# Kernel optimization log

Hardware: AMD Instinct MI355X
Metric: run time of the kernel (lower is better)

The kernel has to match this reference:

```python
import jax, jax.numpy as jnp
import numpy as np


def _scan(xs, w, shift):
    """Sequential IRNN scan.
    xs: [L, B, C, K] - scan over leading axis L.
    shift: 0 = straight scan; +1 = previous line shifted right along K
    (diagonal toward increasing K); -1 = shifted left.
    First line is passed through unchanged (matches torch in-place code).
    """
    def step(carry, row):
        if shift == 0:
            new = jax.nn.relu(carry * w + row)
        elif shift == 1:
            new = jnp.concatenate(
                [row[..., :1], jax.nn.relu(carry[..., :-1] * w + row[..., 1:])], axis=-1)
        else:  # shift == -1
            new = jnp.concatenate(
                [jax.nn.relu(carry[..., 1:] * w + row[..., :-1]), row[..., -1:]], axis=-1)
        return new, new
    _, ys = jax.lax.scan(step, xs[0], xs[1:])
    return jnp.concatenate([xs[:1], ys], axis=0)


def setup_inputs() -> dict:
    key = jax.random.key(0)
    B, C, H, W = 8, 32, 256, 256
    x = jax.random.normal(key, (B, C, H, W), dtype=jnp.float32)
    one = jnp.float32(1.0)
    return {"x": x, "w_up": one, "w_down": one, "w_left": one, "w_right": one}


def reference(x, w_up, w_down, w_left, w_right):
    # Row-major view: [H, B, C, W]
    x_rows = jnp.moveaxis(x, 2, 0)
    top_down = jnp.moveaxis(_scan(x_rows, w_down, 0), 0, 2)
    top_up = jnp.moveaxis(
        jnp.flip(_scan(jnp.flip(x_rows, 0), w_up, 0), 0), 0, 2)
    # Diagonals use w_down, faithful to the original source (which reuses
    # self.down_weight for all four diagonal scans).
    top_zuoxia = jnp.moveaxis(_scan(x_rows, w_down, 1), 0, 2)
    top_youxia = jnp.moveaxis(_scan(x_rows, w_down, -1), 0, 2)

    # Column-major view: [W, B, C, H]
    x_cols = jnp.moveaxis(x, 3, 0)
    top_right = jnp.moveaxis(_scan(x_cols, w_right, 0), 0, 3)
    top_left = jnp.moveaxis(
        jnp.flip(_scan(jnp.flip(x_cols, 0), w_left, 0), 0), 0, 3)
    top_zuoshang = jnp.moveaxis(_scan(x_cols, w_down, 1), 0, 3)
    top_youshang = jnp.moveaxis(_scan(x_cols, w_down, -1), 0, 3)

    return (top_up, top_right, top_down, top_left,
            top_zuoxia, top_youxia, top_zuoshang, top_youshang)
```

## Files before the change

kernel.cpp:

```cpp
#include <hip/hip_runtime.h>


namespace {
constexpr int HH = 256;
constexpr int WW = 256;
constexpr int PLANE = HH * WW;
constexpr size_t TEN = (size_t)PLANE * 256;

__device__ __forceinline__ float relu_f(float a) { return fmaxf(a, 0.0f); }

typedef float v4f __attribute__((ext_vector_type(4)));

__device__ __forceinline__ void nt_store4(float* p, const float4& v) {
    v4f t; t.x = v.x; t.y = v.y; t.z = v.z; t.w = v.w;
    __builtin_nontemporal_store(t, (v4f*)p);
}

__device__ __forceinline__ float4 ld4(const float* p) { return *(const float4*)p; }

template <typename F>
__device__ __forceinline__ void scan_fwd(const float* xp, F&& step) {
    float4 buf[8];
    #pragma unroll
    for (int k = 0; k < 8; ++k) buf[k] = ld4(xp + (1 + k) * WW);
    #pragma unroll 1
    for (int g = 0; g < 30; ++g) {
        #pragma unroll
        for (int k = 0; k < 8; ++k) {
            const int r = 1 + 8 * g + k;
            float4 v = buf[k];
            buf[k] = ld4(xp + (r + 8) * WW);
            step(r, v);
        }
    }
    float4 t7[7];
    #pragma unroll
    for (int k = 0; k < 7; ++k) t7[k] = ld4(xp + (249 + k) * WW);
    #pragma unroll
    for (int k = 0; k < 8; ++k) step(241 + k, buf[k]);
    #pragma unroll
    for (int k = 0; k < 7; ++k) step(249 + k, t7[k]);
}

template <typename F>
__device__ __forceinline__ void scan_bwd(const float* xp, F&& step) {
    float4 buf[8];
    #pragma unroll
    for (int k = 0; k < 8; ++k) buf[k] = ld4(xp + (254 - k) * WW);
    #pragma unroll 1
    for (int g = 0; g < 30; ++g) {
        #pragma unroll
        for (int k = 0; k < 8; ++k) {
            const int h = 254 - (8 * g + k);
            float4 v = buf[k];
            buf[k] = ld4(xp + (h - 8) * WW);
            step(h, v);
        }
    }
    float4 t7[7];
    #pragma unroll
    for (int k = 0; k < 7; ++k) t7[k] = ld4(xp + (6 - k) * WW);
    #pragma unroll
    for (int k = 0; k < 8; ++k) step(14 - k, buf[k]);
    #pragma unroll
    for (int k = 0; k < 7; ++k) step(6 - k, t7[k]);
}
}

__global__ __launch_bounds__(64) void irnn_vertical(
    const float* __restrict__ x, float* __restrict__ out,
    const float* __restrict__ wup_p, const float* __restrict__ wdn_p)
{
    const int bid = blockIdx.x;
    const int t = threadIdx.x;

    if (bid < 256) {
        const int plane = bid;
        const float wd = *wdn_p;
        const float* xp = x + (size_t)plane * PLANE + t * 4;
        float* o2 = out + 2 * TEN + (size_t)plane * PLANE + t * 4;
        float* o4 = out + 4 * TEN + (size_t)plane * PLANE + t * 4;
        float* o5 = out + 5 * TEN + (size_t)plane * PLANE + t * 4;
        float* o6 = out + 6 * TEN + (size_t)plane * PLANE + t * 4;

        float4 c2 = ld4(xp);
        float4 c4 = c2, c5 = c2;
        nt_store4(o2, c2);
        nt_store4(o4, c4);
        nt_store4(o6, c4);
        nt_store4(o5, c5);

        scan_fwd(xp, [&](int r, float4 v) {
            c2.x = relu_f(c2.x * wd + v.x);
            c2.y = relu_f(c2.y * wd + v.y);
            c2.z = relu_f(c2.z * wd + v.z);
            c2.w = relu_f(c2.w * wd + v.w);
            nt_store4(o2 + r * WW, c2);
            {
                float pw = __shfl_up(c4.w, 1);
                float4 n;
                n.x = (t == 0) ? v.x : relu_f(pw * wd + v.x);
                n.y = relu_f(c4.x * wd + v.y);
                n.z = relu_f(c4.y * wd + v.z);
                n.w = relu_f(c4.z * wd + v.w);
                nt_store4(o4 + r * WW, n);
                nt_store4(o6 + r * WW, n);
                c4 = n;
            }
            {
                float nx = __shfl_down(c5.x, 1);
                float4 n;
                n.x = relu_f(c5.y * wd + v.x);
                n.y = relu_f(c5.z * wd + v.y);
                n.z = relu_f(c5.w * wd + v.z);
                n.w = (t == 63) ? v.w : relu_f(nx * wd + v.w);
                nt_store4(o5 + r * WW, n);
                c5 = n;
            }
        });
    } else {
        const int plane = bid - 256;
        const float wu = *wup_p;
        const float wd = *wdn_p;
        const float* xp = x + (size_t)plane * PLANE + t * 4;
        float* o0 = out + 0 * TEN + (size_t)plane * PLANE + t * 4;
        float* o7 = out + 7 * TEN + (size_t)plane * PLANE + t * 4;

        float4 c0 = ld4(xp + 255 * WW);
        float4 c7 = c0;
        nt_store4(o0 + 255 * WW, c0);
        nt_store4(o7 + 255 * WW, c7);

        scan_bwd(xp, [&](int h, float4 v) {
            c0.x = relu_f(c0.x * wu + v.x);
            c0.y = relu_f(c0.y * wu + v.y);
            c0.z = relu_f(c0.z * wu + v.z);
            c0.w = relu_f(c0.w * wu + v.w);
            nt_store4(o0 + h * WW, c0);
            {
                float pw = __shfl_up(c7.w, 1);
                float4 n;
                n.x = (t == 0) ? v.x : relu_f(pw * wd + v.x);
                n.y = relu_f(c7.x * wd + v.y);
                n.z = relu_f(c7.y * wd + v.z);
                n.w = relu_f(c7.z * wd + v.w);
                nt_store4(o7 + h * WW, n);
                c7 = n;
            }
        });
    }
}

__global__ __launch_bounds__(64) void irnn_horizontal(
    const float* __restrict__ x, float* __restrict__ out,
    const float* __restrict__ wlf_p, const float* __restrict__ wrt_p)
{
    __shared__ float xs[64][33];
    __shared__ float os[64][33];

    const int bid = blockIdx.x;
    const int dir = bid >> 10;
    const int rb  = bid & 1023;
    const size_t row0 = (size_t)rb * 64;
    const int t = threadIdx.x;
    const int lrow = t >> 3;
    const int lcol = (t & 7) * 4;

    const float w = dir ? *wlf_p : *wrt_p;
    float* op = out + (size_t)(dir ? 3 : 1) * TEN;

    float carry = 0.0f;
    for (int ci = 0; ci < 8; ++ci) {
        const int cw = dir ? (7 - ci) : ci;
        const int wbase = cw * 32;

        for (int p = 0; p < 8; ++p) {
            const int r = p * 8 + lrow;
            float4 v = *(const float4*)(x + (row0 + r) * WW + wbase + lcol);
            *(float4*)&xs[r][lcol] = v;
        }
        __syncthreads();

        if (dir == 0) {
            for (int j = 0; j < 32; ++j) {
                const float v = xs[t][j];
                const int wg = wbase + j;
                const float o = (wg == 0) ? v : relu_f(carry * w + v);
                carry = o;
                os[t][j] = o;
            }
        } else {
            for (int j = 31; j >= 0; --j) {
                const float v = xs[t][j];
                const int wg = wbase + j;
                const float o = (wg == WW - 1) ? v : relu_f(carry * w + v);
                carry = o;
                os[t][j] = o;
            }
        }
        __syncthreads();

        for (int p = 0; p < 8; ++p) {
            const int r = p * 8 + lrow;
            float4 v = *(const float4*)&os[r][lcol];
            nt_store4(op + (row0 + r) * WW + wbase + lcol, v);
        }
        __syncthreads();
    }
}

extern "C" void kernel_launch(void* const* d_in, const int* in_sizes, int n_in,
                              void* d_out, int out_size, void* d_ws, size_t ws_size,
                              hipStream_t stream) {
    const float* x      = (const float*)d_in[0];
    const float* w_up   = (const float*)d_in[1];
    const float* w_down = (const float*)d_in[2];
    const float* w_left = (const float*)d_in[3];
    const float* w_right= (const float*)d_in[4];
    float* out = (float*)d_out;

    hipLaunchKernelGGL(irnn_vertical, dim3(512), dim3(64), 0, stream,
                       x, out, w_up, w_down);
    hipLaunchKernelGGL(irnn_horizontal, dim3(2 * 1024), dim3(64), 0, stream,
                       x, out, w_left, w_right);
}
```

Before: 118.5 us.

## Fuse horizontal scans into vertical kernel via wave-level parallel prefix scan

Removes the separate horizontal kernel and computes left/right row scans inside the backward vertical blocks, using a lane-parallel prefix scan over each row built from composed affine-ReLU operators exchanged by shuffles. This avoids a second pass reading x and a second launch with shared-memory transposes. In exchange each row step gains many shuffles and extra ALU work on a latency-bound loop, and only 512 single-wave blocks carry all the work.

```diff
diff --git a/kernel.cpp b/kernel.cpp
--- a/kernel.cpp
+++ b/kernel.cpp
@@ -65,11 +65,84 @@
     #pragma unroll
     for (int k = 0; k < 7; ++k) step(6 - k, t7[k]);
 }
-}
-
-__global__ __launch_bounds__(64) void irnn_vertical(
+
+__device__ __forceinline__ float4 wscan_right(float4 v, float k, int t) {
+    float L, K, B;
+    if (t == 0) {
+        float o1 = relu_f(k * v.x + v.y);
+        float o2 = relu_f(k * o1 + v.z);
+        float o3 = relu_f(k * o2 + v.w);
+        L = o3; K = 0.0f; B = o3;
+    } else {
+        L = 0.0f; K = k; B = v.x;
+        L = fmaxf(0.0f, k * L + v.y); B = k * B + v.y; K = k * K;
+        L = fmaxf(0.0f, k * L + v.z); B = k * B + v.z; K = k * K;
+        L = fmaxf(0.0f, k * L + v.w); B = k * B + v.w; K = k * K;
+    }
+    #pragma unroll
+    for (int d = 1; d < 64; d <<= 1) {
+        float Lp = __shfl_up(L, d);
+        float Kp = __shfl_up(K, d);
+        float Bp = __shfl_up(B, d);
+        if (t >= d) {
+            float nL = fmaxf(L, K * Lp + B);
+            float nB = K * Bp + B;
+            float nK = K * Kp;
+            L = nL; B = nB; K = nK;
+        }
+    }
+    float Le = __shfl_up(L, 1);
+    float Be = __shfl_up(B, 1);
+    float c  = fmaxf(Le, Be);
+    float4 o;
+    o.x = (t == 0) ? v.x : relu_f(k * c + v.x);
+    o.y = relu_f(k * o.x + v.y);
+    o.z = relu_f(k * o.y + v.z);
+    o.w = relu_f(k * o.z + v.w);
+    return o;
+}
+
+__device__ __forceinline__ float4 wscan_left(float4 v, float k, int t) {
+    float L, K, B;
+    if (t == 63) {
+        float o2 = relu_f(k * v.w + v.z);
+        float o1 = relu_f(k * o2 + v.y);
+        float o0 = relu_f(k * o1 + v.x);
+        L = o0; K = 0.0f; B = o0;
+    } else {
+        L = 0.0f; K = k; B = v.w;
+        L = fmaxf(0.0f, k * L + v.z); B = k * B + v.z; K = k * K;
+        L = fmaxf(0.0f, k * L + v.y); B = k * B + v.y; K = k * K;
+        L = fmaxf(0.0f, k * L + v.x); B = k * B + v.x; K = k * K;
+    }
+    #pragma unroll
+    for (int d = 1; d < 64; d <<= 1) {
+        float Lp = __shfl_down(L, d);
+        float Kp = __shfl_down(K, d);
+        float Bp = __shfl_down(B, d);
+        if (t < 64 - d) {
+            float nL = fmaxf(L, K * Lp + B);
+            float nB = K * Bp + B;
+            float nK = K * Kp;
+            L = nL; B = nB; K = nK;
+        }
+    }
+    float Le = __shfl_down(L, 1);
+    float Be = __shfl_down(B, 1);
+    float c  = fmaxf(Le, Be);
+    float4 o;
+    o.w = (t == 63) ? v.w : relu_f(k * c + v.w);
+    o.z = relu_f(k * o.w + v.z);
+    o.y = relu_f(k * o.z + v.y);
+    o.x = relu_f(k * o.y + v.x);
+    return o;
+}
+}
+
+__global__ __launch_bounds__(64) void irnn_fused(
     const float* __restrict__ x, float* __restrict__ out,
-    const float* __restrict__ wup_p, const float* __restrict__ wdn_p)
+    const float* __restrict__ wup_p, const float* __restrict__ wdn_p,
+    const float* __restrict__ wlf_p, const float* __restrict__ wrt_p)
 {
     const int bid = blockIdx.x;
     const int t = threadIdx.x;
@@ -122,14 +195,21 @@
         const int plane = bid - 256;
         const float wu = *wup_p;
         const float wd = *wdn_p;
+        const float wr = *wrt_p;
+        const float wl = *wlf_p;
         const float* xp = x + (size_t)plane * PLANE + t * 4;
         float* o0 = out + 0 * TEN + (size_t)plane * PLANE + t * 4;
+        float* o1 = out + 1 * TEN + (size_t)plane * PLANE + t * 4;
+        float* o3 = out + 3 * TEN + (size_t)plane * PLANE + t * 4;
         float* o7 = out + 7 * TEN + (size_t)plane * PLANE + t * 4;
 
-        float4 c0 = ld4(xp + 255 * WW);
-        float4 c7 = c0;
+        float4 v255 = ld4(xp + 255 * WW);
+        float4 c0 = v255;
+        float4 c7 = v255;
         nt_store4(o0 + 255 * WW, c0);
         nt_store4(o7 + 255 * WW, c7);
+        nt_store4(o1 + 255 * WW, wscan_right(v255, wr, t));
+        nt_store4(o3 + 255 * WW, wscan_left(v255, wl, t));
 
         scan_bwd(xp, [&](int h, float4 v) {
             c0.x = relu_f(c0.x * wu + v.x);
@@ -147,65 +227,9 @@
                 nt_store4(o7 + h * WW, n);
                 c7 = n;
             }
+            nt_store4(o1 + h * WW, wscan_right(v, wr, t));
+            nt_store4(o3 + h * WW, wscan_left(v, wl, t));
         });
-    }
-}
-
-__global__ __launch_bounds__(64) void irnn_horizontal(
-    const float* __restrict__ x, float* __restrict__ out,
-    const float* __restrict__ wlf_p, const float* __restrict__ wrt_p)
-{
-    __shared__ float xs[64][33];
-    __shared__ float os[64][33];
-
-    const int bid = blockIdx.x;
-    const int dir = bid >> 10;
-    const int rb  = bid & 1023;
-    const size_t row0 = (size_t)rb * 64;
-    const int t = threadIdx.x;
-    const int lrow = t >> 3;
-    const int lcol = (t & 7) * 4;
-
-    const float w = dir ? *wlf_p : *wrt_p;
-    float* op = out + (size_t)(dir ? 3 : 1) * TEN;
-
-    float carry = 0.0f;
-    for (int ci = 0; ci < 8; ++ci) {
-        const int cw = dir ? (7 - ci) : ci;
-        const int wbase = cw * 32;
-
-        for (int p = 0; p < 8; ++p) {
-            const int r = p * 8 + lrow;
-            float4 v = *(const float4*)(x + (row0 + r) * WW + wbase + lcol);
-            *(float4*)&xs[r][lcol] = v;
-        }
-        __syncthreads();
-
-        if (dir == 0) {
-            for (int j = 0; j < 32; ++j) {
-                const float v = xs[t][j];
-                const int wg = wbase + j;
-                const float o = (wg == 0) ? v : relu_f(carry * w + v);
-                carry = o;
-                os[t][j] = o;
-            }
-        } else {
-            for (int j = 31; j >= 0; --j) {
-                const float v = xs[t][j];
-                const int wg = wbase + j;
-                const float o = (wg == WW - 1) ? v : relu_f(carry * w + v);
-                carry = o;
-                os[t][j] = o;
-            }
-        }
-        __syncthreads();
-
-        for (int p = 0; p < 8; ++p) {
-            const int r = p * 8 + lrow;
-            float4 v = *(const float4*)&os[r][lcol];
-            nt_store4(op + (row0 + r) * WW + wbase + lcol, v);
-        }
-        __syncthreads();
     }
 }
 
@@ -219,8 +243,6 @@
     const float* w_right= (const float*)d_in[4];
     float* out = (float*)d_out;
 
-    hipLaunchKernelGGL(irnn_vertical, dim3(512), dim3(64), 0, stream,
-                       x, out, w_up, w_down);
-    hipLaunchKernelGGL(irnn_horizontal, dim3(2 * 1024), dim3(64), 0, stream,
-                       x, out, w_left, w_right);
-}
+    hipLaunchKernelGGL(irnn_fused, dim3(512), dim3(64), 0, stream,
+                       x, out, w_up, w_down, w_left, w_right);
+}
```

Result: slower. 224.1 us (+89.1%).
